# Kernel tuning notes

Measured on AMD Instinct MI355X. Metric: run time of the kernel, lower is better.

## Reference

```python
import jax, jax.numpy as jnp
import numpy as np
import math

NUM_Q_HEADS = 32
NUM_KV_HEADS = 8


def setup_inputs() -> dict:
    key = jax.random.key(0)
    k1, k2, k3 = jax.random.split(key, 3)
    B, S, E = 2, 2048, 2048
    kv_E = NUM_KV_HEADS * (E // NUM_Q_HEADS)  # 512
    q = jax.random.normal(k1, (B, S, E), dtype=jnp.float32)
    k = jax.random.normal(k2, (B, S, kv_E), dtype=jnp.float32)
    v = jax.random.normal(k3, (B, S, kv_E), dtype=jnp.float32)
    return {"q": q, "k": k, "v": v}


def reference(q, k, v):
    B, S, E = q.shape
    H, KV = NUM_Q_HEADS, NUM_KV_HEADS
    D = E // H
    G = H // KV  # query heads per kv head
    scale = math.sqrt(D)
    # q heads laid out so group g of kv-head h corresponds to q-head h*G+g,
    # matching torch repeat_interleave semantics.
    qh = q.reshape(B, S, KV, G, D).transpose(0, 2, 3, 1, 4)  # [B,KV,G,S,D]
    kh = k.reshape(B, S, KV, D).transpose(0, 2, 1, 3)        # [B,KV,S,D]
    vh = v.reshape(B, S, KV, D).transpose(0, 2, 1, 3)        # [B,KV,S,D]
    scores = jnp.einsum('bkgsd,bktd->bkgst', qh, kh) / scale  # [B,KV,G,S,S]
    weights = jax.nn.softmax(scores, axis=-1)
    out = jnp.einsum('bkgst,bktd->bkgsd', weights, vh)        # [B,KV,G,S,D]
    # back to [B,S,E] with head order (kv_head, group) == q-head index
    return out.transpose(0, 3, 1, 2, 4).reshape(B, S, E)
```

## Files before the change

### kernel.cpp

```cpp
#include <hip/hip_runtime.h>
#include <hip/hip_bf16.h>


#define S_LEN 2048
#define E_DIM 2048
#define KV_E  512
#define D_HEAD 64
#define BN 64
#define NTILE (S_LEN / BN)

typedef __attribute__((ext_vector_type(8))) short short8;
typedef __attribute__((ext_vector_type(4))) float floatx4;
typedef __attribute__((ext_vector_type(4))) unsigned int uint4v;

__device__ __forceinline__ short bf(float x) {
    return __builtin_bit_cast(short, __float2bfloat16(x));
}
__device__ __forceinline__ unsigned cvtpk(float lo, float hi) {
    unsigned r;
    asm("v_cvt_pk_bf16_f32 %0, %1, %2" : "=v"(r) : "v"(lo), "v"(hi));
    return r;
}
__device__ __forceinline__ float vexp2(float x) {
    float r;
    asm("v_exp_f32 %0, %1" : "=v"(r) : "v"(x));
    return r;
}

__global__ __launch_bounds__(256)
void gqa_prepack_kernel(const float* __restrict__ k, const float* __restrict__ v,
                        short* __restrict__ ws) {
    __shared__ float kf[BN][D_HEAD + 2];
    __shared__ float vf[BN][D_HEAD + 2];
    const int kt = blockIdx.x, kvh = blockIdx.y, b = blockIdx.z;
    const int tid = threadIdx.x;
    short* wt = ws + ((size_t)(b * 8 + kvh) * NTILE + kt) * 8192;
    const float* kb = k + ((size_t)(b * S_LEN + kt * BN)) * KV_E + kvh * D_HEAD;
    const float* vb = v + ((size_t)(b * S_LEN + kt * BN)) * KV_E + kvh * D_HEAD;

    #pragma unroll
    for (int i = tid; i < 1024; i += 256) {
        const int r = i >> 4, c0 = (i & 15) << 2;
        floatx4 k4 = *((const floatx4*)(kb + (size_t)r * KV_E + c0));
        floatx4 v4 = *((const floatx4*)(vb + (size_t)r * KV_E + c0));
        kf[r][c0] = k4[0]; kf[r][c0 + 1] = k4[1]; kf[r][c0 + 2] = k4[2]; kf[r][c0 + 3] = k4[3];
        vf[r][c0] = v4[0]; vf[r][c0 + 1] = v4[1]; vf[r][c0 + 2] = v4[2]; vf[r][c0 + 3] = v4[3];
    }
    __syncthreads();
    #pragma unroll
    for (int c = tid; c < 1024; c += 256) {
        const int fk = c >> 6, l = c & 63;
        const int quad = l >> 4, lc = l & 15;
        const int ks = (fk >> 2) & 1, sub = fk & 3;
        short8 s;
        if (fk < 8) {
            const int row = ((lc >> 2) << 3) + (lc & 3) + ((sub & 1) << 2) + ((sub >> 1) << 5);
            const int c0 = ks * 32 + quad * 8;
            #pragma unroll
            for (int j = 0; j < 8; ++j) s[j] = bf(kf[row][c0 + j]);
        } else {
            const int d = sub * 16 + lc;
            const int k0 = ks * 32 + quad * 8;
            #pragma unroll
            for (int j = 0; j < 8; ++j) s[j] = bf(vf[k0 + j][d]);
        }
        *((short8*)(wt + c * 8)) = s;
    }
}

__global__ __launch_bounds__(256, 4)
void GroupedQueryAttention_36163624632989_kernel(
        const float* __restrict__ q,
        const short* __restrict__ ws,
        float* __restrict__ out, const int B) {
    __shared__ short lds[2 * 8192];

    const int f = blockIdx.x;
    const int chunk = gridDim.x >> 3;
    const int wg = (f & 7) * chunk + (f >> 3);
    const int qt = wg & 31;
    const int t2 = wg >> 5;
    const int b  = t2 % B;
    const int hp = t2 / B;
    const int kvh = hp >> 1;

    const int tid  = threadIdx.x;
    const int w    = tid >> 6;
    const int lane = tid & 63;
    const int quad = lane >> 4;
    const int lc   = lane & 15;

    const int h = (hp << 1) + (w & 1);
    const int rowhalf = w >> 1;

    const float SCL = 1.4426950408889634f / 8.0f;

    const short ONE = (short)0x3F80;
    const short8 ones8 = {ONE, ONE, ONE, ONE, ONE, ONE, ONE, ONE};

    short8 aq[2][2];
    #pragma unroll
    for (int mt = 0; mt < 2; ++mt) {
        const int qrow = qt * 64 + rowhalf * 32 + mt * 16 + lc;
        const float* qp = q + ((size_t)(b * S_LEN + qrow)) * E_DIM + h * D_HEAD;
        #pragma unroll
        for (int ks = 0; ks < 2; ++ks) {
            const float* p = qp + ks * 32 + quad * 8;
            floatx4 qa = *((const floatx4*)p);
            floatx4 qb = *((const floatx4*)(p + 4));
            aq[mt][ks][0] = bf(qa[0] * SCL); aq[mt][ks][1] = bf(qa[1] * SCL);
            aq[mt][ks][2] = bf(qa[2] * SCL); aq[mt][ks][3] = bf(qa[3] * SCL);
            aq[mt][ks][4] = bf(qb[0] * SCL); aq[mt][ks][5] = bf(qb[1] * SCL);
            aq[mt][ks][6] = bf(qb[2] * SCL); aq[mt][ks][7] = bf(qb[3] * SCL);
        }
    }

    floatx4 o_acc[2][4];
    floatx4 accL[2];
    #pragma unroll
    for (int mt = 0; mt < 2; ++mt) {
        accL[mt] = (floatx4){0.f, 0.f, 0.f, 0.f};
        #pragma unroll
        for (int i = 0; i < 4; ++i)
            o_acc[mt][i] = (floatx4){0.f, 0.f, 0.f, 0.f};
    }

    const short* wsT = ws + (size_t)(b * 8 + kvh) * NTILE * 8192;

    auto stage = [&](int buf, int kt) {
        const short* src = wsT + (size_t)kt * 8192 + w * 2048 + (lane << 3);
        short* dst = lds + buf * 8192 + w * 2048;
        #pragma unroll
        for (int i = 0; i < 4; ++i)
            __builtin_amdgcn_global_load_lds(
                (const __attribute__((address_space(1))) void*)(src + i * 512),
                (__attribute__((address_space(3))) void*)(dst + i * 512),
                16, 0, 0);
    };

    stage(0, 0);
    __syncthreads();
    int cur = 0;

    for (int kt = 0; kt < NTILE; ++kt) {
        if (kt + 1 < NTILE) stage(cur ^ 1, kt + 1);

        const short* fb = lds + cur * 8192 + (lane << 3);

        floatx4 accT[2][4];
        #pragma unroll
        for (int mt = 0; mt < 2; ++mt)
            #pragma unroll
            for (int t = 0; t < 4; ++t)
                accT[mt][t] = (floatx4){0.f, 0.f, 0.f, 0.f};
        #pragma unroll
        for (int ks = 0; ks < 2; ++ks) {
            short8 bk4[4];
            #pragma unroll
            for (int t = 0; t < 4; ++t)
                bk4[t] = *((const short8*)(fb + (ks * 4 + t) * 512));
            __builtin_amdgcn_s_setprio(1);
            #pragma unroll
            for (int mt = 0; mt < 2; ++mt)
                #pragma unroll
                for (int t = 0; t < 4; ++t)
                    accT[mt][t] = __builtin_amdgcn_mfma_f32_16x16x32_bf16(
                        bk4[t], aq[mt][ks], accT[mt][t], 0, 0, 0);
            __builtin_amdgcn_s_setprio(0);
        }

        #pragma unroll
        for (int ks = 0; ks < 2; ++ks) {
            short8 bv4[4];
            #pragma unroll
            for (int nt = 0; nt < 4; ++nt)
                bv4[nt] = *((const short8*)(fb + (8 + ks * 4 + nt) * 512));
            #pragma unroll
            for (int mt = 0; mt < 2; ++mt) {
                float e0[4], e1[4];
                #pragma unroll
                for (int r = 0; r < 4; ++r) {
                    e0[r] = vexp2(accT[mt][2 * ks][r]);
                    e1[r] = vexp2(accT[mt][2 * ks + 1][r]);
                }
                const unsigned a0 = cvtpk(e0[0], e0[1]);
                const unsigned a1 = cvtpk(e0[2], e0[3]);
                const unsigned a2 = cvtpk(e1[0], e1[1]);
                const unsigned a3 = cvtpk(e1[2], e1[3]);
                const short8 ap = __builtin_bit_cast(short8, (uint4v){a0, a1, a2, a3});
                __builtin_amdgcn_s_setprio(1);
                #pragma unroll
                for (int nt = 0; nt < 4; ++nt)
                    o_acc[mt][nt] = __builtin_amdgcn_mfma_f32_16x16x32_bf16(
                        ap, bv4[nt], o_acc[mt][nt], 0, 0, 0);
                accL[mt] = __builtin_amdgcn_mfma_f32_16x16x32_bf16(
                    ap, ones8, accL[mt], 0, 0, 0);
                __builtin_amdgcn_s_setprio(0);
            }
        }

        __syncthreads();
        cur ^= 1;
    }

    #pragma unroll
    for (int mt = 0; mt < 2; ++mt) {
        float* op = out + (size_t)b * S_LEN * E_DIM + h * D_HEAD;
        #pragma unroll
        for (int r = 0; r < 4; ++r) {
            const float inv_l = 1.0f / accL[mt][r];
            const int grow = qt * 64 + rowhalf * 32 + mt * 16 + quad * 4 + r;
            #pragma unroll
            for (int nt = 0; nt < 4; ++nt)
                op[(size_t)grow * E_DIM + nt * 16 + lc] = o_acc[mt][nt][r] * inv_l;
        }
    }
}

extern "C" void kernel_launch(void* const* d_in, const int* in_sizes, int n_in,
                              void* d_out, int out_size, void* d_ws, size_t ws_size,
                              hipStream_t stream) {
    const float* q = (const float*)d_in[0];
    const float* k = (const float*)d_in[1];
    const float* v = (const float*)d_in[2];
    float* out = (float*)d_out;
    short* ws = (short*)d_ws;
    const int B = in_sizes[0] / (S_LEN * E_DIM);

    dim3 pgrid(NTILE, 8, B);
    gqa_prepack_kernel<<<pgrid, 256, 0, stream>>>(k, v, ws);

    dim3 grid(B * 512);
    GroupedQueryAttention_36163624632989_kernel<<<grid, 256, 0, stream>>>(q, ws, out, B);
}
```

Measured before the change: 153.9 us.

## Software-pipeline QK and PV across m-tiles with triple-buffered V in LDS

Splits the LDS tile into separate K (double-buffered) and V (triple-buffered) regions. The loop is restructured so the QK^T product for one m-tile is interleaved with the exp/PV work of the other m-tile from the previous tile. The goal is to overlap MFMA work with the exp and convert work and cut dependency stalls. In exchange it uses more LDS (40KB vs 32KB), which may reduce occupancy, and the control flow becomes more complex.

```diff
diff --git a/kernel.cpp b/kernel.cpp
--- a/kernel.cpp
+++ b/kernel.cpp
@@ -73,7 +73,9 @@
         const float* __restrict__ q,
         const short* __restrict__ ws,
         float* __restrict__ out, const int B) {
-    __shared__ short lds[2 * 8192];
+    __shared__ short lds[2 * 4096 + 3 * 4096];
+    short* ldsK = lds;
+    short* ldsV = lds + 2 * 4096;
 
     const int f = blockIdx.x;
     const int chunk = gridDim.x >> 3;
@@ -127,81 +129,102 @@
 
     const short* wsT = ws + (size_t)(b * 8 + kvh) * NTILE * 8192;
 
-    auto stage = [&](int buf, int kt) {
-        const short* src = wsT + (size_t)kt * 8192 + w * 2048 + (lane << 3);
-        short* dst = lds + buf * 8192 + w * 2048;
-        #pragma unroll
-        for (int i = 0; i < 4; ++i)
+    auto stageKV = [&](int kbuf, int vbuf, int kt) {
+        const short* srcK = wsT + (size_t)kt * 8192 + w * 1024 + (lane << 3);
+        short* dstK = ldsK + kbuf * 4096 + w * 1024;
+        #pragma unroll
+        for (int i = 0; i < 2; ++i)
             __builtin_amdgcn_global_load_lds(
-                (const __attribute__((address_space(1))) void*)(src + i * 512),
-                (__attribute__((address_space(3))) void*)(dst + i * 512),
+                (const __attribute__((address_space(1))) void*)(srcK + i * 512),
+                (__attribute__((address_space(3))) void*)(dstK + i * 512),
+                16, 0, 0);
+        const short* srcV = wsT + (size_t)kt * 8192 + 4096 + w * 1024 + (lane << 3);
+        short* dstV = ldsV + vbuf * 4096 + w * 1024;
+        #pragma unroll
+        for (int i = 0; i < 2; ++i)
+            __builtin_amdgcn_global_load_lds(
+                (const __attribute__((address_space(1))) void*)(srcV + i * 512),
+                (__attribute__((address_space(3))) void*)(dstV + i * 512),
                 16, 0, 0);
     };
 
-    stage(0, 0);
-    __syncthreads();
-    int cur = 0;
-
-    for (int kt = 0; kt < NTILE; ++kt) {
-        if (kt + 1 < NTILE) stage(cur ^ 1, kt + 1);
-
-        const short* fb = lds + cur * 8192 + (lane << 3);
-
-        floatx4 accT[2][4];
-        #pragma unroll
-        for (int mt = 0; mt < 2; ++mt)
-            #pragma unroll
-            for (int t = 0; t < 4; ++t)
-                accT[mt][t] = (floatx4){0.f, 0.f, 0.f, 0.f};
+    auto qk_mt = [&](const short* fbK, const short8 (&aqm)[2], floatx4 (&acc)[4]) {
+        #pragma unroll
+        for (int t = 0; t < 4; ++t) acc[t] = (floatx4){0.f, 0.f, 0.f, 0.f};
         #pragma unroll
         for (int ks = 0; ks < 2; ++ks) {
-            short8 bk4[4];
-            #pragma unroll
-            for (int t = 0; t < 4; ++t)
-                bk4[t] = *((const short8*)(fb + (ks * 4 + t) * 512));
             __builtin_amdgcn_s_setprio(1);
             #pragma unroll
-            for (int mt = 0; mt < 2; ++mt)
-                #pragma unroll
-                for (int t = 0; t < 4; ++t)
-                    accT[mt][t] = __builtin_amdgcn_mfma_f32_16x16x32_bf16(
-                        bk4[t], aq[mt][ks], accT[mt][t], 0, 0, 0);
+            for (int t = 0; t < 4; ++t) {
+                short8 bk = *((const short8*)(fbK + (ks * 4 + t) * 512));
+                acc[t] = __builtin_amdgcn_mfma_f32_16x16x32_bf16(
+                    bk, aqm[ks], acc[t], 0, 0, 0);
+            }
             __builtin_amdgcn_s_setprio(0);
         }
-
+    };
+
+    auto finish = [&](const floatx4 (&sT)[4], const short* fbV,
+                      floatx4 (&oac)[4], floatx4& aL) {
         #pragma unroll
         for (int ks = 0; ks < 2; ++ks) {
             short8 bv4[4];
             #pragma unroll
             for (int nt = 0; nt < 4; ++nt)
-                bv4[nt] = *((const short8*)(fb + (8 + ks * 4 + nt) * 512));
-            #pragma unroll
-            for (int mt = 0; mt < 2; ++mt) {
-                float e0[4], e1[4];
-                #pragma unroll
-                for (int r = 0; r < 4; ++r) {
-                    e0[r] = vexp2(accT[mt][2 * ks][r]);
-                    e1[r] = vexp2(accT[mt][2 * ks + 1][r]);
-                }
-                const unsigned a0 = cvtpk(e0[0], e0[1]);
-                const unsigned a1 = cvtpk(e0[2], e0[3]);
-                const unsigned a2 = cvtpk(e1[0], e1[1]);
-                const unsigned a3 = cvtpk(e1[2], e1[3]);
-                const short8 ap = __builtin_bit_cast(short8, (uint4v){a0, a1, a2, a3});
-                __builtin_amdgcn_s_setprio(1);
-                #pragma unroll
-                for (int nt = 0; nt < 4; ++nt)
-                    o_acc[mt][nt] = __builtin_amdgcn_mfma_f32_16x16x32_bf16(
-                        ap, bv4[nt], o_acc[mt][nt], 0, 0, 0);
-                accL[mt] = __builtin_amdgcn_mfma_f32_16x16x32_bf16(
-                    ap, ones8, accL[mt], 0, 0, 0);
-                __builtin_amdgcn_s_setprio(0);
+                bv4[nt] = *((const short8*)(fbV + (ks * 4 + nt) * 512));
+            float e0[4], e1[4];
+            #pragma unroll
+            for (int r = 0; r < 4; ++r) {
+                e0[r] = vexp2(sT[2 * ks][r]);
+                e1[r] = vexp2(sT[2 * ks + 1][r]);
             }
-        }
+            const unsigned a0 = cvtpk(e0[0], e0[1]);
+            const unsigned a1 = cvtpk(e0[2], e0[3]);
+            const unsigned a2 = cvtpk(e1[0], e1[1]);
+            const unsigned a3 = cvtpk(e1[2], e1[3]);
+            const short8 ap = __builtin_bit_cast(short8, (uint4v){a0, a1, a2, a3});
+            __builtin_amdgcn_s_setprio(1);
+            #pragma unroll
+            for (int nt = 0; nt < 4; ++nt)
+                oac[nt] = __builtin_amdgcn_mfma_f32_16x16x32_bf16(
+                    ap, bv4[nt], oac[nt], 0, 0, 0);
+            aL = __builtin_amdgcn_mfma_f32_16x16x32_bf16(ap, ones8, aL, 0, 0, 0);
+            __builtin_amdgcn_s_setprio(0);
+        }
+    };
+
+    floatx4 accA[4], accB[4];
+
+    stageKV(0, 0, 0);
+    __syncthreads();
+    stageKV(1, 1, 1);
+    {
+        const short* fbK = ldsK + (lane << 3);
+        const short* fbV = ldsV + (lane << 3);
+        qk_mt(fbK, aq[0], accA);
+        qk_mt(fbK, aq[1], accB);
+        finish(accA, fbV, o_acc[0], accL[0]);
+    }
+    __syncthreads();
+    int vprev = 0, vcur = 1;
+
+    for (int kt = 1; kt < NTILE; ++kt) {
+        const int vnext = (vcur == 2) ? 0 : vcur + 1;
+        if (kt + 1 < NTILE) stageKV((kt + 1) & 1, vnext, kt + 1);
+
+        const short* fbK  = ldsK + (kt & 1) * 4096 + (lane << 3);
+        const short* fbVp = ldsV + vprev * 4096 + (lane << 3);
+        const short* fbVc = ldsV + vcur * 4096 + (lane << 3);
+
+        qk_mt(fbK, aq[0], accA);
+        finish(accB, fbVp, o_acc[1], accL[1]);
+        qk_mt(fbK, aq[1], accB);
+        finish(accA, fbVc, o_acc[0], accL[0]);
 
         __syncthreads();
-        cur ^= 1;
-    }
+        vprev = vcur; vcur = vnext;
+    }
+    finish(accB, ldsV + vprev * 4096 + (lane << 3), o_acc[1], accL[1]);
 
     #pragma unroll
     for (int mt = 0; mt < 2; ++mt) {
```

New measurement: 162.6 us. 5.6% more time.
